# Optimization experiments

Hardware: AMD Instinct MI355X
Metric: run time of the kernel (lower is better)

## Reference

```python
import jax, jax.numpy as jnp
import numpy as np

N_NEURONS = 256
P_MAX = 8
N_BLOCKS = P_MAX + 1
HIDDEN = 32
BATCH = 8192


def setup_inputs() -> dict:
    key = jax.random.key(0)
    ks = jax.random.split(key, 9)
    z = jax.random.normal(ks[0], (BATCH, N_BLOCKS * N_NEURONS), dtype=jnp.float32)
    # Per-block ScalarMLP params, stacked over the n_blocks axis.
    s1 = 1.0 / np.sqrt(N_NEURONS)
    s2 = 1.0 / np.sqrt(HIDDEN)
    gW1 = jax.random.uniform(ks[1], (N_BLOCKS, N_NEURONS, HIDDEN), jnp.float32, -s1, s1)
    gb1 = jax.random.uniform(ks[2], (N_BLOCKS, HIDDEN), jnp.float32, -s1, s1)
    gW2 = jax.random.uniform(ks[3], (N_BLOCKS, HIDDEN, HIDDEN), jnp.float32, -s2, s2)
    gb2 = jax.random.uniform(ks[4], (N_BLOCKS, HIDDEN), jnp.float32, -s2, s2)
    gW3 = jax.random.uniform(ks[5], (N_BLOCKS, HIDDEN), jnp.float32, -s2, s2)
    gb3 = jax.random.uniform(ks[6], (N_BLOCKS,), jnp.float32, -s2, s2)
    # Lag coupling matrices W_r ~ U(-init_scale, init_scale), init_scale=0.1
    W = jax.random.uniform(ks[7], (P_MAX, N_NEURONS, N_NEURONS), jnp.float32, -0.1, 0.1)
    return {"z": z, "gW1": gW1, "gb1": gb1, "gW2": gW2, "gb2": gb2,
            "gW3": gW3, "gb3": gb3, "W": W}


def _energy(z, gW1, gb1, gW2, gb2, gW3, gb3, W):
    B = z.shape[0]
    blocks = z.reshape(B, N_BLOCKS, N_NEURONS)           # (B, K, n)
    # Per-block ScalarMLP energies (all blocks at once).
    h1 = jax.nn.silu(jnp.einsum('bkn,knh->bkh', blocks, gW1) + gb1)   # (B, K, H)
    h2 = jax.nn.silu(jnp.einsum('bkh,khg->bkg', h1, gW2) + gb2)       # (B, K, H)
    e = jnp.einsum('bkh,kh->bk', h2, gW3) + gb3                        # (B, K)
    # Bilinear lag couplings: z_future^T W_r z_{lag-r}, r = 1..p_max.
    z_future = blocks[:, P_MAX, :]                                     # (B, n)
    lags = blocks[:, :P_MAX, :][:, ::-1, :]                            # (B, p, n), index r-1 == block p_max-r
    cross = jnp.einsum('bi,rij,brj->b', z_future, W, lags)             # (B,)
    return e.sum(axis=-1) + cross                                      # (B,)


def reference(z, gW1, gb1, gW2, gb2, gW3, gb3, W):
    # Score s(z) = -grad_z U(z); sum over batch gives per-sample grads
    # since energies are independent across samples.
    grad_z = jax.grad(lambda zz: _energy(zz, gW1, gb1, gW2, gb2, gW3, gb3, W).sum())(z)
    return -grad_z
```

## Files before the change

kernel.cpp:

```cpp
#include <hip/hip_runtime.h>
#include <hip/hip_bf16.h>
#include <math.h>

#define BATCH 8192
#define NB 9
#define NN 256
#define PMAX 8
#define HID 32
#define ZDIM 2304

typedef short bf16x8 __attribute__((ext_vector_type(8)));
typedef float f32x4 __attribute__((ext_vector_type(4)));

static __device__ inline unsigned short f2bf(float f) {
    __hip_bfloat16 h = __float2bfloat16(f);
    return *reinterpret_cast<unsigned short*>(&h);
}

static __device__ inline uint4 pack8(float4 a, float4 b) {
    uint4 u;
    u.x = (unsigned)f2bf(a.x) | ((unsigned)f2bf(a.y) << 16);
    u.y = (unsigned)f2bf(a.z) | ((unsigned)f2bf(a.w) << 16);
    u.z = (unsigned)f2bf(b.x) | ((unsigned)f2bf(b.y) << 16);
    u.w = (unsigned)f2bf(b.z) | ((unsigned)f2bf(b.w) << 16);
    return u;
}

__global__ __launch_bounds__(256) void k_pack(
    const float* __restrict__ W, const float* __restrict__ gW1,
    unsigned short* __restrict__ Wf, unsigned short* __restrict__ WTb,
    unsigned short* __restrict__ gW1b, unsigned short* __restrict__ g1Tb) {
    int r = blockIdx.z;
    int t = threadIdx.x;
    if (r < 8) {
        __shared__ float tt[32][33];
        int i0 = blockIdx.y * 32;
        int j0 = blockIdx.x * 32;
        int tx = t & 31;
        int ty = t >> 5;
        const float* src = W + (size_t)r * 65536;
        int kc2b = ((7 - r) << 3) + (j0 >> 5);
        int j = j0 + tx;
        #pragma unroll
        for (int s = 0; s < 32; s += 8) {
            int i = i0 + ty + s;
            float v = src[(size_t)i * 256 + j];
            tt[ty + s][tx] = v;
            size_t widx = ((size_t)(kc2b * 16 + (i >> 4)) * 64
                           + ((i & 15) + 16 * ((j >> 3) & 3))) * 8 + (j & 7);
            Wf[widx] = f2bf(v);
        }
        __syncthreads();
        #pragma unroll
        for (int s = 0; s < 32; s += 8)
            WTb[(size_t)r * 65536 + (size_t)(j0 + ty + s) * 256 + (i0 + tx)] = f2bf(tt[tx][ty + s]);
    } else {
        int tg = (blockIdx.y * 8 + blockIdx.x) * 256 + t;
        for (int e = tg; e < 73728; e += 16384) {
            float v = gW1[e];
            unsigned short b = f2bf(v);
            gW1b[e] = b;
            int k = e >> 13, n = (e >> 5) & 255, h = e & 31;
            g1Tb[(size_t)(k * 32 + h) * 256 + n] = b;
        }
    }
}

__global__ __launch_bounds__(256) void k_mlp(
    const float* __restrict__ z, const unsigned short* __restrict__ g1Tb,
    const float* __restrict__ gb1, const float* __restrict__ gW2,
    const float* __restrict__ gb2, const float* __restrict__ gW3,
    float* __restrict__ d1ws, unsigned short* __restrict__ zf) {
    __shared__ uint4 As4[2][512];
    __shared__ uint4 Bw[1024];
    __shared__ uint4 W2Ts4[128];
    __shared__ uint4 W2Ns4[128];

    int t = threadIdx.x;
    int lane = t & 63;
    int w = t >> 6;
    int k = blockIdx.y;
    int b0 = blockIdx.x * 128;
    uint4* zfu = (uint4*)zf;
    int rb0 = b0 >> 4;

    const unsigned short* bsrc = g1Tb + (size_t)k * 8192;
    for (int e = t; e < 1024; e += 256) {
        int h = e >> 5;
        int rest = e & 31;
        int c = rest >> 2, qq = rest & 3;
        Bw[c * 128 + (h & 15) + 16 * qq + 64 * (h >> 4)] =
            *(const uint4*)(bsrc + (size_t)h * 256 + c * 32 + qq * 8);
    }
    const float* gw2 = gW2 + (size_t)k * 1024;
    unsigned short* w2t = (unsigned short*)W2Ts4;
    unsigned short* w2n = (unsigned short*)W2Ns4;
    for (int e = t; e < 1024; e += 256) {
        int n = e >> 5, kk = e & 31;
        int qq = kk >> 3, jj = kk & 7;
        int ci = (n & 15) + 16 * qq + 64 * (n >> 4);
        w2t[ci * 8 + jj] = f2bf(gw2[kk * 32 + n]);
        w2n[ci * 8 + jj] = f2bf(gw2[n * 32 + kk]);
    }

    int mq = t >> 2;
    int q = t & 3;
    int ci0 = (mq & 15) + 16 * q + 64 * (mq >> 4);

    f32x4 acc1[2][2];
    #pragma unroll
    for (int i = 0; i < 2; ++i)
        #pragma unroll
        for (int j = 0; j < 2; ++j) acc1[i][j] = (f32x4){0.f, 0.f, 0.f, 0.f};

    auto loadZ = [&](int c, float4 (&fa)[2][2]) {
        #pragma unroll
        for (int pp = 0; pp < 2; ++pp) {
            int m = mq + 64 * pp;
            const float* as = z + (size_t)(b0 + m) * ZDIM + k * 256 + c * 32 + q * 8;
            fa[pp][0] = *(const float4*)(as);
            fa[pp][1] = *(const float4*)(as + 4);
        }
    };
    auto sinkZ = [&](int buf, int c, float4 (&fa)[2][2]) {
        int kc = k * 8 + c;
        #pragma unroll
        for (int pp = 0; pp < 2; ++pp) {
            uint4 pk = pack8(fa[pp][0], fa[pp][1]);
            int ci = ci0 + 256 * pp;
            As4[buf][ci] = pk;
            zfu[((size_t)(rb0 + (ci >> 6)) * 72 + kc) * 64 + (ci & 63)] = pk;
        }
    };

    {
        float4 fa[2][2];
        loadZ(0, fa);
        sinkZ(0, 0, fa);
    }
    int cur = 0;
    for (int c = 0; c < 8; ++c) {
        __syncthreads();
        float4 fan[2][2];
        if (c < 7) loadZ(c + 1, fan);
        bf16x8 af[2], bfr[2];
        #pragma unroll
        for (int i = 0; i < 2; ++i) af[i] = __builtin_bit_cast(bf16x8, As4[cur][lane + (w * 2 + i) * 64]);
        #pragma unroll
        for (int j = 0; j < 2; ++j) bfr[j] = __builtin_bit_cast(bf16x8, Bw[c * 128 + lane + j * 64]);
        #pragma unroll
        for (int i = 0; i < 2; ++i)
            #pragma unroll
            for (int j = 0; j < 2; ++j)
                acc1[i][j] = __builtin_amdgcn_mfma_f32_16x16x32_bf16(af[i], bfr[j], acc1[i][j], 0, 0, 0);
        if (c < 7) sinkZ(cur ^ 1, c + 1, fan);
        cur ^= 1;
    }

    int cq = lane >> 4;
    int ci16 = lane & 15;
    float b1v[2], b2v[2], g3v[2];
    #pragma unroll
    for (int j = 0; j < 2; ++j) {
        b1v[j] = gb1[k * 32 + j * 16 + ci16];
        b2v[j] = gb2[k * 32 + j * 16 + ci16];
        g3v[j] = gW3[k * 32 + j * 16 + ci16];
    }
    unsigned short* Hs = (unsigned short*)As4;
    float sp1[2][2][4];
    __syncthreads();
    #pragma unroll
    for (int i = 0; i < 2; ++i)
        #pragma unroll
        for (int j = 0; j < 2; ++j)
            #pragma unroll
            for (int r = 0; r < 4; ++r) {
                float a1 = acc1[i][j][r] + b1v[j];
                float s1 = 1.f / (1.f + __expf(-a1));
                sp1[i][j][r] = s1 * (1.f + a1 * (1.f - s1));
                int row = w * 32 + i * 16 + cq * 4 + r;
                int col = j * 16 + ci16;
                int chunk = (row & 15) + 16 * (col >> 3) + 64 * (row >> 4);
                Hs[chunk * 8 + (col & 7)] = f2bf(a1 * s1);
            }
    __syncthreads();

    bf16x8 af2[2], wf[2];
    #pragma unroll
    for (int i = 0; i < 2; ++i) af2[i] = __builtin_bit_cast(bf16x8, As4[0][lane + (w * 2 + i) * 64]);
    #pragma unroll
    for (int j = 0; j < 2; ++j) wf[j] = __builtin_bit_cast(bf16x8, W2Ts4[lane + j * 64]);
    f32x4 acc2[2][2];
    #pragma unroll
    for (int i = 0; i < 2; ++i)
        #pragma unroll
        for (int j = 0; j < 2; ++j) {
            acc2[i][j] = (f32x4){0.f, 0.f, 0.f, 0.f};
            acc2[i][j] = __builtin_amdgcn_mfma_f32_16x16x32_bf16(af2[i], wf[j], acc2[i][j], 0, 0, 0);
        }

    __syncthreads();
    #pragma unroll
    for (int i = 0; i < 2; ++i)
        #pragma unroll
        for (int j = 0; j < 2; ++j)
            #pragma unroll
            for (int r = 0; r < 4; ++r) {
                float a2 = acc2[i][j][r] + b2v[j];
                float s2 = 1.f / (1.f + __expf(-a2));
                float da2 = g3v[j] * s2 * (1.f + a2 * (1.f - s2));
                int row = w * 32 + i * 16 + cq * 4 + r;
                int col = j * 16 + ci16;
                int chunk = (row & 15) + 16 * (col >> 3) + 64 * (row >> 4);
                Hs[chunk * 8 + (col & 7)] = f2bf(da2);
            }
    __syncthreads();

    bf16x8 af3[2], wg[2];
    #pragma unroll
    for (int i = 0; i < 2; ++i) af3[i] = __builtin_bit_cast(bf16x8, As4[0][lane + (w * 2 + i) * 64]);
    #pragma unroll
    for (int j = 0; j < 2; ++j) wg[j] = __builtin_bit_cast(bf16x8, W2Ns4[lane + j * 64]);
    #pragma unroll
    for (int i = 0; i < 2; ++i)
        #pragma unroll
        for (int j = 0; j < 2; ++j) {
            f32x4 a3 = (f32x4){0.f, 0.f, 0.f, 0.f};
            a3 = __builtin_amdgcn_mfma_f32_16x16x32_bf16(af3[i], wg[j], a3, 0, 0, 0);
            #pragma unroll
            for (int r = 0; r < 4; ++r) {
                int row = w * 32 + i * 16 + cq * 4 + r;
                int col = j * 16 + ci16;
                d1ws[((size_t)k * BATCH + b0 + row) * 32 + col] = a3[r] * sp1[i][j][r];
            }
        }
}

__global__ __launch_bounds__(256) void k_gemm_lo(
    const unsigned short* __restrict__ zf, const float* __restrict__ d1,
    const unsigned short* __restrict__ WTb, const unsigned short* __restrict__ gW1b,
    float* __restrict__ out) {
    __shared__ uint4 As4[2][512];
    __shared__ uint4 Bs4[2][512];

    int t = threadIdx.x;
    int lane = t & 63;
    int w = t >> 6;
    int wr = w >> 1, wc = w & 1;
    int b0 = blockIdx.x * 128;
    int n0 = blockIdx.y * 128;
    int k  = n0 >> 8;
    int jb = n0 & 255;

    const uint4* zfu = (const uint4*)zf;
    int rb0 = b0 >> 4;
    const float* Aext  = d1 + ((size_t)k * BATCH + b0) * 32;
    const unsigned short* Bmain = WTb + (size_t)(7 - k) * 65536 + (size_t)jb * 256;
    const unsigned short* Bext  = gW1b + ((size_t)k * 256 + jb) * 32;

    int mq = t >> 2;
    int q  = t & 3;
    int ci0 = (mq & 15) + 16 * q + 64 * (mq >> 4);

    auto loadAB = [&](int c, uint4 (&au)[2], uint4 (&bu)[2]) {
        #pragma unroll
        for (int pp = 0; pp < 2; ++pp) {
            int m = mq + 64 * pp;
            int ci = ci0 + 256 * pp;
            if (c < 8) {
                au[pp] = zfu[((size_t)(rb0 + (ci >> 6)) * 72 + 64 + c) * 64 + (ci & 63)];
                bu[pp] = *(const uint4*)(Bmain + (size_t)m * 256 + c * 32 + q * 8);
            } else {
                const float* as = Aext + (size_t)m * 32 + q * 8;
                au[pp] = pack8(*(const float4*)(as), *(const float4*)(as + 4));
                bu[pp] = *(const uint4*)(Bext + (size_t)m * 32 + q * 8);
            }
        }
    };
    auto storeAB = [&](int buf, uint4 (&au)[2], uint4 (&bu)[2]) {
        #pragma unroll
        for (int pp = 0; pp < 2; ++pp) {
            int idx = ci0 + 256 * pp;
            As4[buf][idx] = au[pp];
            Bs4[buf][idx] = bu[pp];
        }
    };

    f32x4 acc[4][4];
    #pragma unroll
    for (int i = 0; i < 4; ++i)
        #pragma unroll
        for (int j = 0; j < 4; ++j) acc[i][j] = (f32x4){0.f, 0.f, 0.f, 0.f};

    {
        uint4 au[2], bu[2];
        loadAB(0, au, bu);
        storeAB(0, au, bu);
    }
    int cur = 0;
    for (int c = 0; c < 9; ++c) {
        __syncthreads();
        uint4 aun[2], bun[2];
        if (c < 8) loadAB(c + 1, aun, bun);
        bf16x8 af[4], bf[4];
        #pragma unroll
        for (int i = 0; i < 4; ++i) af[i] = __builtin_bit_cast(bf16x8, As4[cur][lane + (wr * 4 + i) * 64]);
        #pragma unroll
        for (int j = 0; j < 4; ++j) bf[j] = __builtin_bit_cast(bf16x8, Bs4[cur][lane + (wc * 4 + j) * 64]);
        #pragma unroll
        for (int i = 0; i < 4; ++i)
            #pragma unroll
            for (int j = 0; j < 4; ++j)
                acc[i][j] = __builtin_amdgcn_mfma_f32_16x16x32_bf16(af[i], bf[j], acc[i][j], 0, 0, 0);
        if (c < 8) storeAB(cur ^ 1, aun, bun);
        cur ^= 1;
    }

    int rquad = lane >> 4;
    int cidx  = lane & 15;
    #pragma unroll
    for (int i = 0; i < 4; ++i) {
        #pragma unroll
        for (int j = 0; j < 4; ++j) {
            float* o = out + (size_t)(b0 + wr * 64 + i * 16 + rquad * 4) * ZDIM
                     + (k * 256 + jb + wc * 64 + j * 16 + cidx);
            #pragma unroll
            for (int r = 0; r < 4; ++r)
                o[(size_t)r * ZDIM] = -acc[i][j][r];
        }
    }
}

__global__ __launch_bounds__(256) void k_gemm_hi(
    const unsigned short* __restrict__ zf, const float* __restrict__ d1,
    const unsigned short* __restrict__ Wf, const unsigned short* __restrict__ gW1b,
    float* __restrict__ out) {
    int t = threadIdx.x;
    int lane = t & 63;
    int w = t >> 6;
    int b0 = blockIdx.x * 64;
    int i0 = blockIdx.y * 64;

    int rl = lane & 15;
    int kq = lane >> 4;

    int rb = (b0 >> 4) + w;
    const uint4* Abase = (const uint4*)zf + (size_t)rb * 72 * 64 + lane;
    const uint4* Bbase = (const uint4*)Wf + (size_t)(i0 >> 4) * 64 + lane;
    const float* atail = d1 + ((size_t)8 * BATCH + b0 + w * 16 + rl) * 32 + kq * 8;

    f32x4 acc[4];
    #pragma unroll
    for (int j = 0; j < 4; ++j) acc[j] = (f32x4){0.f, 0.f, 0.f, 0.f};

    auto loadA = [&](int c, uint4& x) {
        if (c < 64) x = Abase[(size_t)c * 64];
        else x = pack8(*(const float4*)(atail), *(const float4*)(atail + 4));
    };
    auto loadB = [&](int c, uint4 (&bb)[4]) {
        if (c < 64) {
            #pragma unroll
            for (int j = 0; j < 4; ++j)
                bb[j] = Bbase[(size_t)c * 1024 + j * 64];
        } else {
            #pragma unroll
            for (int j = 0; j < 4; ++j)
                bb[j] = *(const uint4*)(gW1b + (size_t)(8 * 256 + i0 + j * 16 + rl) * 32 + kq * 8);
        }
    };

    uint4 a;
    uint4 bb[4];
    loadA(0, a);
    loadB(0, bb);
    for (int c = 0; c < 65; ++c) {
        uint4 na;
        uint4 nbb[4];
        if (c < 64) {
            loadA(c + 1, na);
            loadB(c + 1, nbb);
        }
        bf16x8 af = __builtin_bit_cast(bf16x8, a);
        #pragma unroll
        for (int j = 0; j < 4; ++j)
            acc[j] = __builtin_amdgcn_mfma_f32_16x16x32_bf16(
                af, __builtin_bit_cast(bf16x8, bb[j]), acc[j], 0, 0, 0);
        if (c < 64) {
            a = na;
            #pragma unroll
            for (int j = 0; j < 4; ++j) bb[j] = nbb[j];
        }
    }

    #pragma unroll
    for (int j = 0; j < 4; ++j) {
        float* o = out + (size_t)(b0 + w * 16 + kq * 4) * ZDIM + 2048 + i0 + j * 16 + rl;
        #pragma unroll
        for (int r = 0; r < 4; ++r)
            o[(size_t)r * ZDIM] = -acc[j][r];
    }
}

extern "C" void kernel_launch(void* const* d_in, const int* in_sizes, int n_in,
                              void* d_out, int out_size, void* d_ws, size_t ws_size,
                              hipStream_t stream) {
    const float* z   = (const float*)d_in[0];
    const float* gW1 = (const float*)d_in[1];
    const float* gb1 = (const float*)d_in[2];
    const float* gW2 = (const float*)d_in[3];
    const float* gb2 = (const float*)d_in[4];
    const float* gW3 = (const float*)d_in[5];
    const float* W   = (const float*)d_in[7];
    float* out = (float*)d_out;

    float* ws = (float*)d_ws;
    float*          d1ws = ws;
    unsigned short* WTb  = (unsigned short*)(ws + 2359296);
    unsigned short* Wf   = WTb + 524288;
    unsigned short* gW1b = Wf + 524288;
    unsigned short* g1Tb = gW1b + 73728;
    unsigned short* zf   = g1Tb + 73728;

    k_pack<<<dim3(8, 8, 9), 256, 0, stream>>>(W, gW1, Wf, WTb, gW1b, g1Tb);
    k_mlp<<<dim3(64, 9), 256, 0, stream>>>(z, g1Tb, gb1, gW2, gb2, gW3, d1ws, zf);
    k_gemm_lo<<<dim3(64, 16), 256, 0, stream>>>(zf, d1ws, WTb, gW1b, out);
    k_gemm_hi<<<dim3(128, 4), 256, 0, stream>>>(zf, d1ws, Wf, gW1b, out);
}
```

Baseline: 204.0 us.

## Halve MLP batch tile and write d1 as packed bf16 fragments

The MLP kernel now processes 64 rows per block instead of 128, doubling grid size to 1152 blocks for more parallelism. The per-block backward activation d1 is written as bf16 in the MFMA-fragment layout via a final LDS staging pass, instead of fp32 row-major. Both GEMM kernels then load d1 fragments directly rather than reading fp32 and packing on the fly. This cuts d1 traffic in half and removes conversion work, at the cost of an extra barrier and LDS round-trip, and it also reloads the weight tiles once per block across twice as many blocks.

```diff
diff --git a/kernel.cpp b/kernel.cpp
--- a/kernel.cpp
+++ b/kernel.cpp
@@ -70,8 +70,8 @@
     const float* __restrict__ z, const unsigned short* __restrict__ g1Tb,
     const float* __restrict__ gb1, const float* __restrict__ gW2,
     const float* __restrict__ gb2, const float* __restrict__ gW3,
-    float* __restrict__ d1ws, unsigned short* __restrict__ zf) {
-    __shared__ uint4 As4[2][512];
+    unsigned short* __restrict__ d1f, unsigned short* __restrict__ zf) {
+    __shared__ uint4 As4[2][256];
     __shared__ uint4 Bw[1024];
     __shared__ uint4 W2Ts4[128];
     __shared__ uint4 W2Ns4[128];
@@ -80,8 +80,9 @@
     int lane = t & 63;
     int w = t >> 6;
     int k = blockIdx.y;
-    int b0 = blockIdx.x * 128;
+    int b0 = blockIdx.x * 64;
     uint4* zfu = (uint4*)zf;
+    uint4* d1fu = (uint4*)d1f;
     int rb0 = b0 >> 4;
 
     const unsigned short* bsrc = g1Tb + (size_t)k * 8192;
@@ -107,52 +108,38 @@
     int q = t & 3;
     int ci0 = (mq & 15) + 16 * q + 64 * (mq >> 4);
 
-    f32x4 acc1[2][2];
-    #pragma unroll
-    for (int i = 0; i < 2; ++i)
-        #pragma unroll
-        for (int j = 0; j < 2; ++j) acc1[i][j] = (f32x4){0.f, 0.f, 0.f, 0.f};
-
-    auto loadZ = [&](int c, float4 (&fa)[2][2]) {
-        #pragma unroll
-        for (int pp = 0; pp < 2; ++pp) {
-            int m = mq + 64 * pp;
-            const float* as = z + (size_t)(b0 + m) * ZDIM + k * 256 + c * 32 + q * 8;
-            fa[pp][0] = *(const float4*)(as);
-            fa[pp][1] = *(const float4*)(as + 4);
-        }
-    };
-    auto sinkZ = [&](int buf, int c, float4 (&fa)[2][2]) {
-        int kc = k * 8 + c;
-        #pragma unroll
-        for (int pp = 0; pp < 2; ++pp) {
-            uint4 pk = pack8(fa[pp][0], fa[pp][1]);
-            int ci = ci0 + 256 * pp;
-            As4[buf][ci] = pk;
-            zfu[((size_t)(rb0 + (ci >> 6)) * 72 + kc) * 64 + (ci & 63)] = pk;
-        }
+    f32x4 acc1[2];
+    #pragma unroll
+    for (int j = 0; j < 2; ++j) acc1[j] = (f32x4){0.f, 0.f, 0.f, 0.f};
+
+    auto loadZ = [&](int c, float4 (&fa)[2]) {
+        const float* as = z + (size_t)(b0 + mq) * ZDIM + k * 256 + c * 32 + q * 8;
+        fa[0] = *(const float4*)(as);
+        fa[1] = *(const float4*)(as + 4);
+    };
+    auto sinkZ = [&](int buf, int c, float4 (&fa)[2]) {
+        uint4 pk = pack8(fa[0], fa[1]);
+        As4[buf][ci0] = pk;
+        zfu[((size_t)(rb0 + (ci0 >> 6)) * 72 + (k * 8 + c)) * 64 + (ci0 & 63)] = pk;
     };
 
     {
-        float4 fa[2][2];
+        float4 fa[2];
         loadZ(0, fa);
         sinkZ(0, 0, fa);
     }
     int cur = 0;
     for (int c = 0; c < 8; ++c) {
         __syncthreads();
-        float4 fan[2][2];
+        float4 fan[2];
         if (c < 7) loadZ(c + 1, fan);
-        bf16x8 af[2], bfr[2];
-        #pragma unroll
-        for (int i = 0; i < 2; ++i) af[i] = __builtin_bit_cast(bf16x8, As4[cur][lane + (w * 2 + i) * 64]);
+        bf16x8 af = __builtin_bit_cast(bf16x8, As4[cur][w * 64 + lane]);
+        bf16x8 bfr[2];
         #pragma unroll
         for (int j = 0; j < 2; ++j) bfr[j] = __builtin_bit_cast(bf16x8, Bw[c * 128 + lane + j * 64]);
         #pragma unroll
-        for (int i = 0; i < 2; ++i)
-            #pragma unroll
-            for (int j = 0; j < 2; ++j)
-                acc1[i][j] = __builtin_amdgcn_mfma_f32_16x16x32_bf16(af[i], bfr[j], acc1[i][j], 0, 0, 0);
+        for (int j = 0; j < 2; ++j)
+            acc1[j] = __builtin_amdgcn_mfma_f32_16x16x32_bf16(af, bfr[j], acc1[j], 0, 0, 0);
         if (c < 7) sinkZ(cur ^ 1, c + 1, fan);
         cur ^= 1;
     }
@@ -167,77 +154,69 @@
         g3v[j] = gW3[k * 32 + j * 16 + ci16];
     }
     unsigned short* Hs = (unsigned short*)As4;
-    float sp1[2][2][4];
-    __syncthreads();
-    #pragma unroll
-    for (int i = 0; i < 2; ++i)
-        #pragma unroll
-        for (int j = 0; j < 2; ++j)
-            #pragma unroll
-            for (int r = 0; r < 4; ++r) {
-                float a1 = acc1[i][j][r] + b1v[j];
-                float s1 = 1.f / (1.f + __expf(-a1));
-                sp1[i][j][r] = s1 * (1.f + a1 * (1.f - s1));
-                int row = w * 32 + i * 16 + cq * 4 + r;
-                int col = j * 16 + ci16;
-                int chunk = (row & 15) + 16 * (col >> 3) + 64 * (row >> 4);
-                Hs[chunk * 8 + (col & 7)] = f2bf(a1 * s1);
-            }
-    __syncthreads();
-
-    bf16x8 af2[2], wf[2];
-    #pragma unroll
-    for (int i = 0; i < 2; ++i) af2[i] = __builtin_bit_cast(bf16x8, As4[0][lane + (w * 2 + i) * 64]);
+    float sp1[2][4];
+    __syncthreads();
+    #pragma unroll
+    for (int j = 0; j < 2; ++j)
+        #pragma unroll
+        for (int r = 0; r < 4; ++r) {
+            float a1 = acc1[j][r] + b1v[j];
+            float s1 = 1.f / (1.f + __expf(-a1));
+            sp1[j][r] = s1 * (1.f + a1 * (1.f - s1));
+            int col = j * 16 + ci16;
+            int chunk = ci16 + 16 * (col >> 3) + 64 * w;
+            chunk = (cq * 4 + r) + 16 * (col >> 3) + 64 * w;
+            Hs[chunk * 8 + (col & 7)] = f2bf(a1 * s1);
+        }
+    __syncthreads();
+
+    bf16x8 af2 = __builtin_bit_cast(bf16x8, As4[0][w * 64 + lane]);
+    bf16x8 wf[2];
     #pragma unroll
     for (int j = 0; j < 2; ++j) wf[j] = __builtin_bit_cast(bf16x8, W2Ts4[lane + j * 64]);
-    f32x4 acc2[2][2];
-    #pragma unroll
-    for (int i = 0; i < 2; ++i)
-        #pragma unroll
-        for (int j = 0; j < 2; ++j) {
-            acc2[i][j] = (f32x4){0.f, 0.f, 0.f, 0.f};
-            acc2[i][j] = __builtin_amdgcn_mfma_f32_16x16x32_bf16(af2[i], wf[j], acc2[i][j], 0, 0, 0);
-        }
-
-    __syncthreads();
-    #pragma unroll
-    for (int i = 0; i < 2; ++i)
-        #pragma unroll
-        for (int j = 0; j < 2; ++j)
-            #pragma unroll
-            for (int r = 0; r < 4; ++r) {
-                float a2 = acc2[i][j][r] + b2v[j];
-                float s2 = 1.f / (1.f + __expf(-a2));
-                float da2 = g3v[j] * s2 * (1.f + a2 * (1.f - s2));
-                int row = w * 32 + i * 16 + cq * 4 + r;
-                int col = j * 16 + ci16;
-                int chunk = (row & 15) + 16 * (col >> 3) + 64 * (row >> 4);
-                Hs[chunk * 8 + (col & 7)] = f2bf(da2);
-            }
-    __syncthreads();
-
-    bf16x8 af3[2], wg[2];
-    #pragma unroll
-    for (int i = 0; i < 2; ++i) af3[i] = __builtin_bit_cast(bf16x8, As4[0][lane + (w * 2 + i) * 64]);
+    f32x4 acc2[2];
+    #pragma unroll
+    for (int j = 0; j < 2; ++j) {
+        acc2[j] = (f32x4){0.f, 0.f, 0.f, 0.f};
+        acc2[j] = __builtin_amdgcn_mfma_f32_16x16x32_bf16(af2, wf[j], acc2[j], 0, 0, 0);
+    }
+
+    __syncthreads();
+    #pragma unroll
+    for (int j = 0; j < 2; ++j)
+        #pragma unroll
+        for (int r = 0; r < 4; ++r) {
+            float a2 = acc2[j][r] + b2v[j];
+            float s2 = 1.f / (1.f + __expf(-a2));
+            float da2 = g3v[j] * s2 * (1.f + a2 * (1.f - s2));
+            int col = j * 16 + ci16;
+            int chunk = (cq * 4 + r) + 16 * (col >> 3) + 64 * w;
+            Hs[chunk * 8 + (col & 7)] = f2bf(da2);
+        }
+    __syncthreads();
+
+    bf16x8 af3 = __builtin_bit_cast(bf16x8, As4[0][w * 64 + lane]);
+    bf16x8 wg[2];
     #pragma unroll
     for (int j = 0; j < 2; ++j) wg[j] = __builtin_bit_cast(bf16x8, W2Ns4[lane + j * 64]);
-    #pragma unroll
-    for (int i = 0; i < 2; ++i)
-        #pragma unroll
-        for (int j = 0; j < 2; ++j) {
-            f32x4 a3 = (f32x4){0.f, 0.f, 0.f, 0.f};
-            a3 = __builtin_amdgcn_mfma_f32_16x16x32_bf16(af3[i], wg[j], a3, 0, 0, 0);
-            #pragma unroll
-            for (int r = 0; r < 4; ++r) {
-                int row = w * 32 + i * 16 + cq * 4 + r;
-                int col = j * 16 + ci16;
-                d1ws[((size_t)k * BATCH + b0 + row) * 32 + col] = a3[r] * sp1[i][j][r];
-            }
-        }
+    __syncthreads();
+    #pragma unroll
+    for (int j = 0; j < 2; ++j) {
+        f32x4 a3 = (f32x4){0.f, 0.f, 0.f, 0.f};
+        a3 = __builtin_amdgcn_mfma_f32_16x16x32_bf16(af3, wg[j], a3, 0, 0, 0);
+        #pragma unroll
+        for (int r = 0; r < 4; ++r) {
+            int col = j * 16 + ci16;
+            int chunk = (cq * 4 + r) + 16 * (col >> 3) + 64 * w;
+            Hs[chunk * 8 + (col & 7)] = f2bf(a3[r] * sp1[j][r]);
+        }
+    }
+    __syncthreads();
+    d1fu[((size_t)k * 512 + rb0 + (t >> 6)) * 64 + (t & 63)] = As4[0][t];
 }
 
 __global__ __launch_bounds__(256) void k_gemm_lo(
-    const unsigned short* __restrict__ zf, const float* __restrict__ d1,
+    const unsigned short* __restrict__ zf, const unsigned short* __restrict__ d1f,
     const unsigned short* __restrict__ WTb, const unsigned short* __restrict__ gW1b,
     float* __restrict__ out) {
     __shared__ uint4 As4[2][512];
@@ -252,9 +231,9 @@
     int k  = n0 >> 8;
     int jb = n0 & 255;
 
-    const uint4* zfu = (const uint4*)zf;
+    const uint4* zfu  = (const uint4*)zf;
+    const uint4* d1fu = (const uint4*)d1f;
     int rb0 = b0 >> 4;
-    const float* Aext  = d1 + ((size_t)k * BATCH + b0) * 32;
     const unsigned short* Bmain = WTb + (size_t)(7 - k) * 65536 + (size_t)jb * 256;
     const unsigned short* Bext  = gW1b + ((size_t)k * 256 + jb) * 32;
 
@@ -271,8 +250,7 @@
                 au[pp] = zfu[((size_t)(rb0 + (ci >> 6)) * 72 + 64 + c) * 64 + (ci & 63)];
                 bu[pp] = *(const uint4*)(Bmain + (size_t)m * 256 + c * 32 + q * 8);
             } else {
-                const float* as = Aext + (size_t)m * 32 + q * 8;
-                au[pp] = pack8(*(const float4*)(as), *(const float4*)(as + 4));
+                au[pp] = d1fu[((size_t)k * 512 + rb0 + (ci >> 6)) * 64 + (ci & 63)];
                 bu[pp] = *(const uint4*)(Bext + (size_t)m * 32 + q * 8);
             }
         }
@@ -332,7 +310,7 @@
 }
 
 __global__ __launch_bounds__(256) void k_gemm_hi(
-    const unsigned short* __restrict__ zf, const float* __restrict__ d1,
+    const unsigned short* __restrict__ zf, const unsigned short* __restrict__ d1f,
     const unsigned short* __restrict__ Wf, const unsigned short* __restrict__ gW1b,
     float* __restrict__ out) {
     int t = threadIdx.x;
@@ -346,16 +324,15 @@
 
     int rb = (b0 >> 4) + w;
     const uint4* Abase = (const uint4*)zf + (size_t)rb * 72 * 64 + lane;
+    const uint4* Atail = (const uint4*)d1f + ((size_t)8 * 512 + rb) * 64 + lane;
     const uint4* Bbase = (const uint4*)Wf + (size_t)(i0 >> 4) * 64 + lane;
-    const float* atail = d1 + ((size_t)8 * BATCH + b0 + w * 16 + rl) * 32 + kq * 8;
 
     f32x4 acc[4];
     #pragma unroll
     for (int j = 0; j < 4; ++j) acc[j] = (f32x4){0.f, 0.f, 0.f, 0.f};
 
     auto loadA = [&](int c, uint4& x) {
-        if (c < 64) x = Abase[(size_t)c * 64];
-        else x = pack8(*(const float4*)(atail), *(const float4*)(atail + 4));
+        x = (c < 64) ? Abase[(size_t)c * 64] : Atail[0];
     };
     auto loadB = [&](int c, uint4 (&bb)[4]) {
         if (c < 64) {
@@ -413,16 +390,15 @@
     const float* W   = (const float*)d_in[7];
     float* out = (float*)d_out;
 
-    float* ws = (float*)d_ws;
-    float*          d1ws = ws;
-    unsigned short* WTb  = (unsigned short*)(ws + 2359296);
+    unsigned short* d1f  = (unsigned short*)d_ws;
+    unsigned short* WTb  = d1f + 2359296;
     unsigned short* Wf   = WTb + 524288;
     unsigned short* gW1b = Wf + 524288;
     unsigned short* g1Tb = gW1b + 73728;
     unsigned short* zf   = g1Tb + 73728;
 
     k_pack<<<dim3(8, 8, 9), 256, 0, stream>>>(W, gW1, Wf, WTb, gW1b, g1Tb);
-    k_mlp<<<dim3(64, 9), 256, 0, stream>>>(z, g1Tb, gb1, gW2, gb2, gW3, d1ws, zf);
-    k_gemm_lo<<<dim3(64, 16), 256, 0, stream>>>(zf, d1ws, WTb, gW1b, out);
-    k_gemm_hi<<<dim3(128, 4), 256, 0, stream>>>(zf, d1ws, Wf, gW1b, out);
-}
+    k_mlp<<<dim3(128, 9), 256, 0, stream>>>(z, g1Tb, gb1, gW2, gb2, gW3, d1f, zf);
+    k_gemm_lo<<<dim3(64, 16), 256, 0, stream>>>(zf, d1f, WTb, gW1b, out);
+    k_gemm_hi<<<dim3(128, 4), 256, 0, stream>>>(zf, d1f, Wf, gW1b, out);
+}
```

Result: no change. 203.1 us (-0.4%).
